# Kernel optimization log

Hardware: AMD Instinct MI355X
Metric: run time of the kernel (lower is better)

The kernel has to match this reference:

```python
import jax, jax.numpy as jnp
import numpy as np

N_ATOMS = 8192
N_PAIRS = 65536
F = 128        # n_atombasis
R = 20         # n_radialbasis
B = 5          # graph_n_blocks
EPS = 1e-8     # stability constant


def setup_inputs() -> dict:
    key = jax.random.key(0)
    ks = jax.random.split(key, 16)
    rn = lambda k, shape, s=0.05: jax.random.normal(k, shape, dtype=jnp.float32) * s
    return {
        "features": jax.random.normal(ks[0], (N_ATOMS, F), jnp.float32),
        "distances": jax.random.uniform(ks[1], (N_PAIRS,), jnp.float32, 0.5, 5.0),
        "vectors": jax.random.normal(ks[2], (N_PAIRS, 3), jnp.float32),
        "cutoffs": jax.random.uniform(ks[3], (N_PAIRS,), jnp.float32),
        "rbfs": jax.random.normal(ks[4], (N_PAIRS, R), jnp.float32),
        "filter_W": rn(ks[5], (R, B * 3 * F)),
        "filter_b": jnp.zeros((B * 3 * F,), jnp.float32),
        "int_W1": rn(ks[6], (B, F, F)),
        "int_b1": jnp.zeros((B, F), jnp.float32),
        "int_W2": rn(ks[7], (B, F, 3 * F)),
        "int_b2": jnp.zeros((B, 3 * F), jnp.float32),
        "mix_Wv": rn(ks[8], (B, F, 2 * F)),
        "mix_W1": rn(ks[9], (B, 2 * F, F)),
        "mix_b1": jnp.zeros((B, F), jnp.float32),
        "mix_W2": rn(ks[10], (B, F, 3 * F)),
        "mix_b2": jnp.zeros((B, 3 * F), jnp.float32),
        "idx_i": jax.random.randint(ks[11], (N_PAIRS,), 0, N_ATOMS),
        "idx_j": jax.random.randint(ks[12], (N_PAIRS,), 0, N_ATOMS),
    }


def reference(features, distances, vectors, cutoffs, rbfs,
              filter_W, filter_b, int_W1, int_b1, int_W2, int_b2,
              mix_Wv, mix_W1, mix_b1, mix_W2, mix_b2, idx_i, idx_j):
    n_atoms = features.shape[0]
    # Cutoff-weighted radial filters, one (3F) chunk per block: [P, B*3F]
    descriptors = (rbfs @ filter_W + filter_b) * cutoffs[:, None]
    dir_ij = vectors / distances[:, None]                       # [P, 3]

    q = features[:, None, :]                                    # [N, 1, F]
    mu = jnp.zeros((n_atoms, 3, F), dtype=features.dtype)       # [N, 3, F]

    for b in range(B):
        # --- interaction block ---
        x = jax.nn.silu(q @ int_W1[b] + int_b1[b]) @ int_W2[b] + int_b2[b]  # [N,1,3F]
        Wij = descriptors[:, None, b * 3 * F:(b + 1) * 3 * F]               # [P,1,3F]
        xj = x[idx_j] * Wij                                                 # [P,1,3F]
        muj = mu[idx_j]                                                     # [P,3,F]
        dq, dmuR, dmumu = jnp.split(xj, 3, axis=-1)                         # [P,1,F] each
        dmu = dmuR * dir_ij[:, :, None] + dmumu * muj                       # [P,3,F]
        q = q + jax.ops.segment_sum(dq, idx_i, num_segments=n_atoms)
        mu = mu + jax.ops.segment_sum(dmu, idx_i, num_segments=n_atoms)

        # --- mixing block ---
        mu_V, mu_W = jnp.split(mu @ mix_Wv[b], 2, axis=-1)                  # [N,3,F] each
        mu_Vn = jnp.sqrt(jnp.sum(mu_V ** 2, axis=-2, keepdims=True) + EPS)  # [N,1,F]
        ctx = jnp.concatenate([q, mu_Vn], axis=-1)                          # [N,1,2F]
        y = jax.nn.silu(ctx @ mix_W1[b] + mix_b1[b]) @ mix_W2[b] + mix_b2[b]
        dq_i, dmu_i, dqmu_i = jnp.split(y, 3, axis=-1)                      # [N,1,F] each
        q = q + dq_i + dqmu_i * jnp.sum(mu_V * mu_W, axis=1, keepdims=True)
        mu = mu + dmu_i * mu_W

    return q[:, 0, :], mu
```

## Files before the change

### kernel.cpp

```cpp
#include <hip/hip_runtime.h>
#include <hip/hip_bf16.h>

#define NA 8192
#define NP 65536
#define WROW 1920

typedef short short8 __attribute__((ext_vector_type(8)));
typedef short short4v __attribute__((ext_vector_type(4)));
typedef float floatx4 __attribute__((ext_vector_type(4)));

static __device__ __forceinline__ short f2bf(float f) {
    union { float f; unsigned u; } v; v.f = f;
    unsigned r = v.u + 0x7FFF + ((v.u >> 16) & 1);
    return (short)(r >> 16);
}
static __device__ __forceinline__ float bf2f(short s) {
    union { unsigned u; float f; } v;
    v.u = ((unsigned)(unsigned short)s) << 16;
    return v.f;
}
static __device__ __forceinline__ unsigned char f2fp8(float f) {
    int p = __builtin_amdgcn_cvt_pk_fp8_f32(f, 0.f, 0, false);
    return (unsigned char)(p & 0xFF);
}
static __device__ __forceinline__ float fp82f(unsigned char b) {
    return __builtin_amdgcn_cvt_f32_fp8((int)b, 0);
}
static __device__ __forceinline__ float silu(float v) {
    return v / (1.f + __expf(-v));
}

static __device__ __forceinline__ void swz(const float* __restrict__ src,
                                           short* __restrict__ dst,
                                           int K, int N, int idx) {
    int kn = K * N;
    int b = idx / kn;
    int r = idx - b * kn;
    int tile = r >> 9, li = r & 511;
    int lane = li >> 3, bb = li & 7;
    int Kt = K >> 5;
    int nt = tile / Kt, kt = tile - nt * Kt;
    int k = kt * 32 + (lane >> 4) * 8 + bb;
    int n = nt * 16 + (lane & 15);
    dst[idx] = f2bf(src[b * kn + k * N + n]);
}

__global__ __launch_bounds__(256) void k_tconv_all(const float* __restrict__ iW1,
                                                   const float* __restrict__ iW2,
                                                   const float* __restrict__ mWv,
                                                   const float* __restrict__ mW1,
                                                   const float* __restrict__ mW2,
                                                   const float* __restrict__ fW,
                                                   short* __restrict__ W1t,
                                                   short* __restrict__ W2t,
                                                   short* __restrict__ Wvt,
                                                   short* __restrict__ mW1t,
                                                   short* __restrict__ mW2t,
                                                   short* __restrict__ fWt) {
    int idx = blockIdx.x * 256 + threadIdx.x;
    if (idx < 81920)       { swz(iW1, W1t, 128, 128, idx); return; }
    idx -= 81920;
    if (idx < 245760)      { swz(iW2, W2t, 128, 384, idx); return; }
    idx -= 245760;
    if (idx < 163840)      { swz(mWv, Wvt, 128, 256, idx); return; }
    idx -= 163840;
    if (idx < 163840)      { swz(mW1, mW1t, 256, 128, idx); return; }
    idx -= 163840;
    if (idx < 245760)      { swz(mW2, mW2t, 128, 384, idx); return; }
    idx -= 245760;
    if (idx < 61440) {
        int b = idx / 12288;
        int r = idx - b * 12288;
        int nt = r >> 9;
        int li = r & 511;
        int lane = li >> 3, bb = li & 7;
        int k = (lane >> 4) * 8 + bb;
        int n = nt * 16 + (lane & 15);
        fWt[idx] = (k < 20) ? f2bf(fW[k * WROW + b * 384 + n]) : (short)0;
    }
}

__global__ __launch_bounds__(256) void k_init(const float* __restrict__ feat,
                                              float* __restrict__ q,
                                              float* __restrict__ mu,
                                              short* __restrict__ q_bf,
                                              short* __restrict__ mu_bfA,
                                              int* __restrict__ counts,
                                              int* __restrict__ cursor,
                                              float* __restrict__ cut_csr,
                                              short* __restrict__ rbf_c) {
    int idx = blockIdx.x * 256 + threadIdx.x;
    if (idx < NA * 128) { float v = feat[idx]; q[idx] = v; q_bf[idx] = f2bf(v); }
    mu[idx] = 0.f;
    mu_bfA[idx] = 0;
    if (idx < NA) { counts[idx] = 0; cursor[idx] = 0; }
    if (idx < 16) {
        cut_csr[NP + idx] = 0.f;
        #pragma unroll
        for (int k = 0; k < 32; ++k) rbf_c[(NP + idx) * 32 + k] = 0;
    }
}

__global__ __launch_bounds__(256) void k_hist(const int* __restrict__ idx_i,
                                              int* __restrict__ counts) {
    int p = blockIdx.x * 256 + threadIdx.x;
    if (p < NP) atomicAdd(&counts[idx_i[p]], 1);
}

__global__ __launch_bounds__(1024) void k_scan(const int* __restrict__ counts,
                                               int* __restrict__ offs) {
    __shared__ int sums[1024];
    int t = threadIdx.x;
    int local[8];
    int s = 0;
    #pragma unroll
    for (int k = 0; k < 8; ++k) { local[k] = s; s += counts[t * 8 + k]; }
    sums[t] = s;
    __syncthreads();
    for (int off = 1; off < 1024; off <<= 1) {
        int v = sums[t];
        int u = (t >= off) ? sums[t - off] : 0;
        __syncthreads();
        sums[t] = v + u;
        __syncthreads();
    }
    int base = (t > 0) ? sums[t - 1] : 0;
    #pragma unroll
    for (int k = 0; k < 8; ++k) offs[t * 8 + k] = base + local[k];
    if (t == 1023) offs[NA] = sums[1023];
}

__global__ __launch_bounds__(256) void k_fillprep(const int* __restrict__ idx_i,
                                                  const int* __restrict__ idx_j,
                                                  const int* __restrict__ offs,
                                                  int* __restrict__ cursor,
                                                  const float* __restrict__ cut,
                                                  const float* __restrict__ dist,
                                                  const float* __restrict__ vec,
                                                  const float* __restrict__ rbfs,
                                                  int* __restrict__ jcsr,
                                                  float* __restrict__ cut_csr,
                                                  float4* __restrict__ dir_csr,
                                                  short* __restrict__ rbf_c) {
    int p = blockIdx.x * 256 + threadIdx.x;
    if (p >= NP) return;
    int i = idx_i[p];
    int pos = atomicAdd(&cursor[i], 1);
    int e = offs[i] + pos;
    jcsr[e] = idx_j[p];
    float c = cut[p];
    cut_csr[e] = c;
    float invd = 1.f / dist[p];
    float4 d;
    d.x = vec[p * 3 + 0] * invd;
    d.y = vec[p * 3 + 1] * invd;
    d.z = vec[p * 3 + 2] * invd;
    d.w = 0.f;
    dir_csr[e] = d;
    #pragma unroll
    for (int k = 0; k < 20; ++k) rbf_c[e * 32 + k] = f2bf(rbfs[p * 20 + k] * c);
    #pragma unroll
    for (int k = 20; k < 32; ++k) rbf_c[e * 32 + k] = 0;
}

__global__ __launch_bounds__(256) void k_x(const short* __restrict__ q_bf,
                                           const short* __restrict__ W1sw,
                                           const short* __restrict__ W2sw,
                                           const float* __restrict__ b1,
                                           const float* __restrict__ b2,
                                           unsigned char* __restrict__ x_fp8) {
    __shared__ __align__(16) short qtile[16 * 136];
    __shared__ __align__(16) short hs[16 * 136];
    int t = threadIdx.x;
    int wv = t >> 6, lane = t & 63, quad = lane >> 4, l16 = lane & 15;
    int a0 = blockIdx.x * 16;

    #pragma unroll
    for (int it = 0; it < 2; ++it) {
        int c = it * 256 + t;
        int row = c >> 5, col4 = c & 31;
        *(short4v*)(qtile + row * 136 + col4 * 4) =
            *(const short4v*)(q_bf + (a0 + row) * 128 + col4 * 4);
    }
    __syncthreads();

    floatx4 acc0 = {0.f, 0.f, 0.f, 0.f}, acc1 = {0.f, 0.f, 0.f, 0.f};
    #pragma unroll
    for (int kk = 0; kk < 4; ++kk) {
        short8 a  = *(const short8*)(qtile + l16 * 136 + kk * 32 + quad * 8);
        short8 b0 = *(const short8*)(W1sw + ((wv * 2 + 0) * 4 + kk) * 512 + lane * 8);
        short8 bq = *(const short8*)(W1sw + ((wv * 2 + 1) * 4 + kk) * 512 + lane * 8);
        acc0 = __builtin_amdgcn_mfma_f32_16x16x32_bf16(a, b0, acc0, 0, 0, 0);
        acc1 = __builtin_amdgcn_mfma_f32_16x16x32_bf16(a, bq, acc1, 0, 0, 0);
    }
    __syncthreads();
    {
        int n0 = wv * 32 + l16;
        float bia0 = b1[n0], bia1 = b1[n0 + 16];
        #pragma unroll
        for (int r = 0; r < 4; ++r) {
            int m = quad * 4 + r;
            hs[m * 136 + n0]      = f2bf(silu(acc0[r] + bia0));
            hs[m * 136 + n0 + 16] = f2bf(silu(acc1[r] + bia1));
        }
    }
    __syncthreads();
    floatx4 acc[6];
    #pragma unroll
    for (int jj = 0; jj < 6; ++jj) acc[jj] = {0.f, 0.f, 0.f, 0.f};
    #pragma unroll
    for (int kk = 0; kk < 4; ++kk) {
        short8 a = *(const short8*)(hs + l16 * 136 + kk * 32 + quad * 8);
        #pragma unroll
        for (int jj = 0; jj < 6; ++jj) {
            short8 b = *(const short8*)(W2sw + ((wv * 6 + jj) * 4 + kk) * 512 + lane * 8);
            acc[jj] = __builtin_amdgcn_mfma_f32_16x16x32_bf16(a, b, acc[jj], 0, 0, 0);
        }
    }
    #pragma unroll
    for (int jj = 0; jj < 6; ++jj) {
        int n = wv * 96 + jj * 16 + l16;
        float bia = b2[n];
        #pragma unroll
        for (int r = 0; r < 4; ++r) {
            int m = quad * 4 + r;
            x_fp8[(a0 + m) * 384 + n] = f2fp8(acc[jj][r] + bia);
        }
    }
}

__global__ __launch_bounds__(256, 6) void k_gather(const unsigned char* __restrict__ x_fp8,
                                                   const short* __restrict__ mu_bfA,
                                                   const short* __restrict__ rbf_c,
                                                   const short* __restrict__ fWt,
                                                   const float* __restrict__ fbp,
                                                   const int* __restrict__ jcsr,
                                                   const float* __restrict__ cut_csr,
                                                   const float4* __restrict__ dir_csr,
                                                   const int* __restrict__ offs,
                                                   float* __restrict__ q,
                                                   float* __restrict__ mu,
                                                   short* __restrict__ q_bf,
                                                   short* __restrict__ mu_bfB) {
    __shared__ short dlds[16 * 392];
    __shared__ float pm[4 * 128];
    int i = blockIdx.x;
    int t = threadIdx.x;
    int h = t >> 7;
    int f = t & 127;
    int wv = t >> 6, lane = t & 63, quad = lane >> 4, l16 = lane & 15;
    int start = offs[i], end = offs[i + 1];
    float qa = 0.f, m0a = 0.f, m1a = 0.f, m2a = 0.f;

    for (int e0 = start; e0 < end; e0 += 16) {
        if (e0 > start) __syncthreads();
        short8 a = *(const short8*)(rbf_c + (e0 + l16) * 32 + quad * 8);
        float c0 = cut_csr[e0 + quad * 4 + 0];
        float c1 = cut_csr[e0 + quad * 4 + 1];
        float c2 = cut_csr[e0 + quad * 4 + 2];
        float c3 = cut_csr[e0 + quad * 4 + 3];
        #pragma unroll
        for (int nt = 0; nt < 6; ++nt) {
            int col = wv * 96 + nt * 16 + l16;
            short8 bfr = *(const short8*)(fWt + (wv * 6 + nt) * 512 + lane * 8);
            floatx4 z = {0.f, 0.f, 0.f, 0.f};
            floatx4 acc = __builtin_amdgcn_mfma_f32_16x16x32_bf16(a, bfr, z, 0, 0, 0);
            float fbv = fbp[col];
            dlds[(quad * 4 + 0) * 392 + col] = f2bf(acc[0] + fbv * c0);
            dlds[(quad * 4 + 1) * 392 + col] = f2bf(acc[1] + fbv * c1);
            dlds[(quad * 4 + 2) * 392 + col] = f2bf(acc[2] + fbv * c2);
            dlds[(quad * 4 + 3) * 392 + col] = f2bf(acc[3] + fbv * c3);
        }
        __syncthreads();
        int lim = (end < e0 + 16) ? end : (e0 + 16);
        int e = e0 + h;
        if (e < lim) {
            int jA = jcsr[e];
            float4 dirA = dir_csr[e];
            unsigned char aX0 = x_fp8[jA * 384 + f];
            unsigned char aX1 = x_fp8[jA * 384 + 128 + f];
            unsigned char aX2 = x_fp8[jA * 384 + 256 + f];
            short aU0 = mu_bfA[jA * 384 + f];
            short aU1 = mu_bfA[jA * 384 + 128 + f];
            short aU2 = mu_bfA[jA * 384 + 256 + f];
            for (; e < lim; e += 2) {
                float x0 = fp82f(aX0), x1 = fp82f(aX1), x2 = fp82f(aX2);
                float u0 = bf2f(aU0), u1 = bf2f(aU1), u2 = bf2f(aU2);
                float4 cdir = dirA;
                int en = e + 2;
                if (en < lim) {
                    int jn = jcsr[en];
                    dirA = dir_csr[en];
                    aX0 = x_fp8[jn * 384 + f];
                    aX1 = x_fp8[jn * 384 + 128 + f];
                    aX2 = x_fp8[jn * 384 + 256 + f];
                    aU0 = mu_bfA[jn * 384 + f];
                    aU1 = mu_bfA[jn * 384 + 128 + f];
                    aU2 = mu_bfA[jn * 384 + 256 + f];
                }
                int le = e - e0;
                float wa = bf2f(dlds[le * 392 + f]);
                float wb = bf2f(dlds[le * 392 + 128 + f]);
                float wc = bf2f(dlds[le * 392 + 256 + f]);
                qa += x0 * wa;
                float xb = x1 * wb;
                float xc = x2 * wc;
                m0a += xb * cdir.x + xc * u0;
                m1a += xb * cdir.y + xc * u1;
                m2a += xb * cdir.z + xc * u2;
            }
        }
    }
    if (h == 1) {
        pm[0 * 128 + f] = qa;
        pm[1 * 128 + f] = m0a;
        pm[2 * 128 + f] = m1a;
        pm[3 * 128 + f] = m2a;
    }
    __syncthreads();
    if (h == 0) {
        qa  += pm[0 * 128 + f];
        m0a += pm[1 * 128 + f];
        m1a += pm[2 * 128 + f];
        m2a += pm[3 * 128 + f];
        float qn = q[i * 128 + f] + qa;
        q[i * 128 + f] = qn;
        q_bf[i * 128 + f] = f2bf(qn);
        float mn0 = mu[(i * 3 + 0) * 128 + f] + m0a;
        float mn1 = mu[(i * 3 + 1) * 128 + f] + m1a;
        float mn2 = mu[(i * 3 + 2) * 128 + f] + m2a;
        mu[(i * 3 + 0) * 128 + f] = mn0;
        mu[(i * 3 + 1) * 128 + f] = mn1;
        mu[(i * 3 + 2) * 128 + f] = mn2;
        mu_bfB[(i * 3 + 0) * 128 + f] = f2bf(mn0);
        mu_bfB[(i * 3 + 1) * 128 + f] = f2bf(mn1);
        mu_bfB[(i * 3 + 2) * 128 + f] = f2bf(mn2);
    }
}

__global__ __launch_bounds__(512, 4) void k_mixx(const short* __restrict__ mu_bfB,
                                                 const short* __restrict__ Wvsw,
                                                 const short* __restrict__ q_bf_ro,
                                                 const short* __restrict__ W1sw,
                                                 const short* __restrict__ W2sw,
                                                 const float* __restrict__ b1,
                                                 const float* __restrict__ b2,
                                                 float* __restrict__ q,
                                                 float* __restrict__ mu,
                                                 short* __restrict__ q_bf,
                                                 short* __restrict__ mu_bfA,
                                                 const short* __restrict__ xW1sw,
                                                 const short* __restrict__ xW2sw,
                                                 const float* __restrict__ xb1,
                                                 const float* __restrict__ xb2,
                                                 unsigned char* __restrict__ x_fp8,
                                                 int do_x) {
    __shared__ __align__(16) char smem[51968];
    short* ms    = (short*)(smem);
    short* qtile = (short*)(smem + 13056);
    short* Vv    = (short*)(smem + 17408);
    short* hs    = (short*)(smem + 17408);
    short* Vw    = (short*)(smem + 30464);
    short* vnb   = (short*)(smem + 43520);
    short* sb    = (short*)(smem + 47872);
    int t = threadIdx.x;
    int wv = t >> 6, lane = t & 63, quad = lane >> 4, l16 = lane & 15;
    int a0 = blockIdx.x * 16;

    #pragma unroll
    for (int it = 0; it < 3; ++it) {
        int c = it * 512 + t;
        int row = c >> 5, col4 = c & 31;
        *(short4v*)(ms + row * 136 + col4 * 4) =
            *(const short4v*)(mu_bfB + (a0 * 3 + row) * 128 + col4 * 4);
    }
    {
        int row = t >> 5, col4 = t & 31;
        *(short4v*)(qtile + row * 136 + col4 * 4) =
            *(const short4v*)(q_bf_ro + (a0 + row) * 128 + col4 * 4);
    }
    __syncthreads();

    {
        floatx4 acc[3][2];
        #pragma unroll
        for (int mt = 0; mt < 3; ++mt)
            #pragma unroll
            for (int nt = 0; nt < 2; ++nt) acc[mt][nt] = {0.f, 0.f, 0.f, 0.f};
        #pragma unroll
        for (int kk = 0; kk < 4; ++kk) {
            short8 a[3];
            #pragma unroll
            for (int mt = 0; mt < 3; ++mt)
                a[mt] = *(const short8*)(ms + (mt * 16 + l16) * 136 + kk * 32 + quad * 8);
            #pragma unroll
            for (int nt = 0; nt < 2; ++nt) {
                short8 b = *(const short8*)(Wvsw + ((wv * 2 + nt) * 4 + kk) * 512 + lane * 8);
                #pragma unroll
                for (int mt = 0; mt < 3; ++mt)
                    acc[mt][nt] = __builtin_amdgcn_mfma_f32_16x16x32_bf16(a[mt], b, acc[mt][nt], 0, 0, 0);
            }
        }
        __syncthreads();
        #pragma unroll
        for (int mt = 0; mt < 3; ++mt)
            #pragma unroll
            for (int nt = 0; nt < 2; ++nt)
                #pragma unroll
                for (int r = 0; r < 4; ++r) {
                    int row = mt * 16 + quad * 4 + r;
                    int col = wv * 32 + nt * 16 + l16;
                    short v = f2bf(acc[mt][nt][r]);
                    if (col < 128) Vv[row * 136 + col] = v;
                    else           Vw[row * 136 + col - 128] = v;
                }
    }
    __syncthreads();
    #pragma unroll
    for (int k = 0; k < 4; ++k) {
        int idx = k * 512 + t;
        int a = idx >> 7, c = idx & 127;
        float v0 = bf2f(Vv[(a * 3 + 0) * 136 + c]);
        float v1 = bf2f(Vv[(a * 3 + 1) * 136 + c]);
        float v2 = bf2f(Vv[(a * 3 + 2) * 136 + c]);
        float w0 = bf2f(Vw[(a * 3 + 0) * 136 + c]);
        float w1 = bf2f(Vw[(a * 3 + 1) * 136 + c]);
        float w2 = bf2f(Vw[(a * 3 + 2) * 136 + c]);
        vnb[a * 136 + c] = f2bf(sqrtf(v0 * v0 + v1 * v1 + v2 * v2 + 1e-8f));
        sb[a * 128 + c]  = f2bf(v0 * w0 + v1 * w1 + v2 * w2);
    }
    __syncthreads();
    {
        floatx4 acc0 = {0.f, 0.f, 0.f, 0.f};
        #pragma unroll
        for (int kk = 0; kk < 8; ++kk) {
            short8 a;
            if (kk < 4)
                a = *(const short8*)(qtile + l16 * 136 + kk * 32 + quad * 8);
            else
                a = *(const short8*)(vnb + l16 * 136 + (kk - 4) * 32 + quad * 8);
            short8 b0 = *(const short8*)(W1sw + (wv * 8 + kk) * 512 + lane * 8);
            acc0 = __builtin_amdgcn_mfma_f32_16x16x32_bf16(a, b0, acc0, 0, 0, 0);
        }
        __syncthreads();
        int n0 = wv * 16 + l16;
        float bia0 = b1[n0];
        #pragma unroll
        for (int r = 0; r < 4; ++r) {
            int m = quad * 4 + r;
            hs[m * 136 + n0] = f2bf(silu(acc0[r] + bia0));
        }
    }
    __syncthreads();
    {
        floatx4 accB[3];
        #pragma unroll
        for (int c = 0; c < 3; ++c) accB[c] = {0.f, 0.f, 0.f, 0.f};
        #pragma unroll
        for (int kk = 0; kk < 4; ++kk) {
            short8 a = *(const short8*)(hs + l16 * 136 + kk * 32 + quad * 8);
            #pragma unroll
            for (int c = 0; c < 3; ++c) {
                short8 b = *(const short8*)(W2sw + ((c * 8 + wv) * 4 + kk) * 512 + lane * 8);
                accB[c] = __builtin_amdgcn_mfma_f32_16x16x32_bf16(a, b, accB[c], 0, 0, 0);
            }
        }
        int co = wv * 16 + l16;
        float bq_  = b2[co];
        float bm_  = b2[128 + co];
        float bqm_ = b2[256 + co];
        #pragma unroll
        for (int r = 0; r < 4; ++r) {
            int m = quad * 4 + r;
            int ga = a0 + m;
            float dq   = accB[0][r] + bq_;
            float dmu  = accB[1][r] + bm_;
            float dqmu = accB[2][r] + bqm_;
            float sv = bf2f(sb[m * 128 + co]);
            float qn = q[ga * 128 + co] + dq + dqmu * sv;
            q[ga * 128 + co] = qn;
            short qnb = f2bf(qn);
            q_bf[ga * 128 + co] = qnb;
            qtile[m * 136 + co] = qnb;
            #pragma unroll
            for (int d = 0; d < 3; ++d) {
                float mw = bf2f(Vw[(m * 3 + d) * 136 + co]);
                float mn = mu[(ga * 3 + d) * 128 + co] + dmu * mw;
                mu[(ga * 3 + d) * 128 + co] = mn;
                mu_bfA[(ga * 3 + d) * 128 + co] = f2bf(mn);
            }
        }
    }
    if (!do_x) return;
    __syncthreads();
    {
        floatx4 acc0 = {0.f, 0.f, 0.f, 0.f};
        #pragma unroll
        for (int kk = 0; kk < 4; ++kk) {
            short8 a  = *(const short8*)(qtile + l16 * 136 + kk * 32 + quad * 8);
            short8 b0 = *(const short8*)(xW1sw + (wv * 4 + kk) * 512 + lane * 8);
            acc0 = __builtin_amdgcn_mfma_f32_16x16x32_bf16(a, b0, acc0, 0, 0, 0);
        }
        __syncthreads();
        int n0 = wv * 16 + l16;
        float bia0 = xb1[n0];
        #pragma unroll
        for (int r = 0; r < 4; ++r) {
            int m = quad * 4 + r;
            hs[m * 136 + n0] = f2bf(silu(acc0[r] + bia0));
        }
    }
    __syncthreads();
    {
        floatx4 acc[3];
        #pragma unroll
        for (int jj = 0; jj < 3; ++jj) acc[jj] = {0.f, 0.f, 0.f, 0.f};
        #pragma unroll
        for (int kk = 0; kk < 4; ++kk) {
            short8 a = *(const short8*)(hs + l16 * 136 + kk * 32 + quad * 8);
            #pragma unroll
            for (int jj = 0; jj < 3; ++jj) {
                short8 b = *(const short8*)(xW2sw + ((wv * 3 + jj) * 4 + kk) * 512 + lane * 8);
                acc[jj] = __builtin_amdgcn_mfma_f32_16x16x32_bf16(a, b, acc[jj], 0, 0, 0);
            }
        }
        #pragma unroll
        for (int jj = 0; jj < 3; ++jj) {
            int n = wv * 48 + jj * 16 + l16;
            float bia = xb2[n];
            #pragma unroll
            for (int r = 0; r < 4; ++r) {
                int m = quad * 4 + r;
                x_fp8[(a0 + m) * 384 + n] = f2fp8(acc[jj][r] + bia);
            }
        }
    }
}

extern "C" void kernel_launch(void* const* d_in, const int* in_sizes, int n_in,
                              void* d_out, int out_size, void* d_ws, size_t ws_size,
                              hipStream_t stream) {
    const float* feat = (const float*)d_in[0];
    const float* dist = (const float*)d_in[1];
    const float* vec  = (const float*)d_in[2];
    const float* cut  = (const float*)d_in[3];
    const float* rbfs = (const float*)d_in[4];
    const float* fW   = (const float*)d_in[5];
    const float* fb   = (const float*)d_in[6];
    const float* iW1  = (const float*)d_in[7];
    const float* ib1  = (const float*)d_in[8];
    const float* iW2  = (const float*)d_in[9];
    const float* ib2  = (const float*)d_in[10];
    const float* mWv  = (const float*)d_in[11];
    const float* mW1  = (const float*)d_in[12];
    const float* mb1  = (const float*)d_in[13];
    const float* mW2  = (const float*)d_in[14];
    const float* mb2  = (const float*)d_in[15];
    const int* idx_i  = (const int*)d_in[16];
    const int* idx_j  = (const int*)d_in[17];

    float* q  = (float*)d_out;
    float* mu = (float*)d_out + NA * 128;

    char* w = (char*)d_ws;
    unsigned char* x_fp8 = (unsigned char*)(w);
    short* q_bf    = (short*)(w + 6291456);
    short* mu_bfA  = (short*)(w + 8388608);
    short* mu_bfB  = (short*)(w + 14680064);
    short* W1t     = (short*)(w + 20971520);
    short* W2t     = (short*)(w + 21135360);
    short* Wvt     = (short*)(w + 21626880);
    short* mW1t    = (short*)(w + 21954560);
    short* mW2t    = (short*)(w + 22282240);
    short* fWt     = (short*)(w + 22773760);
    int*   counts  = (int*)(w + 22896640);
    int*   cursor  = (int*)(w + 22929408);
    int*   offs    = (int*)(w + 22962176);
    int*   jcsr    = (int*)(w + 23257104);
    float* cut_csr = (float*)(w + 23519248);
    float4* dir_csr= (float4*)(w + 23781456);
    short* rbf_c   = (short*)(w + 24830032);

    k_tconv_all<<<(962560 + 255) / 256, 256, 0, stream>>>(iW1, iW2, mWv, mW1, mW2, fW,
                                                          W1t, W2t, Wvt, mW1t, mW2t, fWt);
    k_init<<<NA * 384 / 256, 256, 0, stream>>>(feat, q, mu, q_bf, mu_bfA, counts, cursor,
                                               cut_csr, rbf_c);
    k_hist<<<NP / 256, 256, 0, stream>>>(idx_i, counts);
    k_scan<<<1, 1024, 0, stream>>>(counts, offs);
    k_fillprep<<<NP / 256, 256, 0, stream>>>(idx_i, idx_j, offs, cursor, cut, dist, vec,
                                             rbfs, jcsr, cut_csr, dir_csr, rbf_c);

    k_x<<<NA / 16, 256, 0, stream>>>(q_bf, W1t, W2t, ib1, ib2, x_fp8);
    for (int b = 0; b < 5; ++b) {
        int bn = (b + 1) % 5;
        k_gather<<<NA, 256, 0, stream>>>(x_fp8, mu_bfA, rbf_c, fWt + b * 12288,
                                         fb + b * 384, jcsr, cut_csr, dir_csr,
                                         offs, q, mu, q_bf, mu_bfB);
        k_mixx<<<NA / 16, 512, 0, stream>>>(mu_bfB, Wvt + b * 32768, q_bf,
                                            mW1t + b * 32768, mW2t + b * 49152,
                                            mb1 + b * 128, mb2 + b * 384,
                                            q, mu, q_bf, mu_bfA,
                                            W1t + bn * 16384, W2t + bn * 49152,
                                            ib1 + bn * 128, ib2 + bn * 384,
                                            x_fp8, (b < 4) ? 1 : 0);
    }
}
```

Measured before the change: 429.0 us.

## Emit bf16 deltas from gather and fold residual update into mixing kernel

The gather kernel no longer reads and writes the fp32 q/mu state and its bf16 copies. It writes only bf16 deltas for q and mu. The mixing kernel now reads the fp32 state plus the deltas, forms the updated tiles itself, and applies the residual in its epilogue. This cuts the gather kernel's read-modify-write traffic, but the mixing kernel reads fp32 state and the deltas twice, and storing the aggregated deltas in bf16 adds rounding error.

```diff
diff --git a/kernel.cpp b/kernel.cpp
--- a/kernel.cpp
+++ b/kernel.cpp
@@ -238,10 +238,8 @@
                                                    const float* __restrict__ cut_csr,
                                                    const float4* __restrict__ dir_csr,
                                                    const int* __restrict__ offs,
-                                                   float* __restrict__ q,
-                                                   float* __restrict__ mu,
-                                                   short* __restrict__ q_bf,
-                                                   short* __restrict__ mu_bfB) {
+                                                   short* __restrict__ dqg,
+                                                   short* __restrict__ dmug) {
     __shared__ short dlds[16 * 392];
     __shared__ float pm[4 * 128];
     int i = blockIdx.x;
@@ -323,31 +321,24 @@
         m0a += pm[1 * 128 + f];
         m1a += pm[2 * 128 + f];
         m2a += pm[3 * 128 + f];
-        float qn = q[i * 128 + f] + qa;
-        q[i * 128 + f] = qn;
-        q_bf[i * 128 + f] = f2bf(qn);
-        float mn0 = mu[(i * 3 + 0) * 128 + f] + m0a;
-        float mn1 = mu[(i * 3 + 1) * 128 + f] + m1a;
-        float mn2 = mu[(i * 3 + 2) * 128 + f] + m2a;
-        mu[(i * 3 + 0) * 128 + f] = mn0;
-        mu[(i * 3 + 1) * 128 + f] = mn1;
-        mu[(i * 3 + 2) * 128 + f] = mn2;
-        mu_bfB[(i * 3 + 0) * 128 + f] = f2bf(mn0);
-        mu_bfB[(i * 3 + 1) * 128 + f] = f2bf(mn1);
-        mu_bfB[(i * 3 + 2) * 128 + f] = f2bf(mn2);
-    }
-}
-
-__global__ __launch_bounds__(512, 4) void k_mixx(const short* __restrict__ mu_bfB,
+        dqg[i * 128 + f]             = f2bf(qa);
+        dmug[(i * 3 + 0) * 128 + f]  = f2bf(m0a);
+        dmug[(i * 3 + 1) * 128 + f]  = f2bf(m1a);
+        dmug[(i * 3 + 2) * 128 + f]  = f2bf(m2a);
+    }
+}
+
+__global__ __launch_bounds__(512, 4) void k_mixx(const float* __restrict__ mu_ro,
+                                                 const short* __restrict__ dmug,
+                                                 const float* __restrict__ q_ro,
+                                                 const short* __restrict__ dqg,
                                                  const short* __restrict__ Wvsw,
-                                                 const short* __restrict__ q_bf_ro,
                                                  const short* __restrict__ W1sw,
                                                  const short* __restrict__ W2sw,
                                                  const float* __restrict__ b1,
                                                  const float* __restrict__ b2,
                                                  float* __restrict__ q,
                                                  float* __restrict__ mu,
-                                                 short* __restrict__ q_bf,
                                                  short* __restrict__ mu_bfA,
                                                  const short* __restrict__ xW1sw,
                                                  const short* __restrict__ xW2sw,
@@ -368,16 +359,18 @@
     int a0 = blockIdx.x * 16;
 
     #pragma unroll
-    for (int it = 0; it < 3; ++it) {
-        int c = it * 512 + t;
-        int row = c >> 5, col4 = c & 31;
-        *(short4v*)(ms + row * 136 + col4 * 4) =
-            *(const short4v*)(mu_bfB + (a0 * 3 + row) * 128 + col4 * 4);
-    }
-    {
-        int row = t >> 5, col4 = t & 31;
-        *(short4v*)(qtile + row * 136 + col4 * 4) =
-            *(const short4v*)(q_bf_ro + (a0 + row) * 128 + col4 * 4);
+    for (int k = 0; k < 12; ++k) {
+        int idx = k * 512 + t;
+        int row = idx >> 7, c = idx & 127;
+        int g = (a0 * 3 + row) * 128 + c;
+        ms[row * 136 + c] = f2bf(mu_ro[g] + bf2f(dmug[g]));
+    }
+    #pragma unroll
+    for (int k = 0; k < 4; ++k) {
+        int idx = k * 512 + t;
+        int row = idx >> 7, c = idx & 127;
+        int g = (a0 + row) * 128 + c;
+        qtile[row * 136 + c] = f2bf(q_ro[g] + bf2f(dqg[g]));
     }
     __syncthreads();
 
@@ -477,17 +470,17 @@
             float dmu  = accB[1][r] + bm_;
             float dqmu = accB[2][r] + bqm_;
             float sv = bf2f(sb[m * 128 + co]);
-            float qn = q[ga * 128 + co] + dq + dqmu * sv;
-            q[ga * 128 + co] = qn;
-            short qnb = f2bf(qn);
-            q_bf[ga * 128 + co] = qnb;
-            qtile[m * 136 + co] = qnb;
+            int gq = ga * 128 + co;
+            float qn = (q[gq] + bf2f(dqg[gq])) + dq + dqmu * sv;
+            q[gq] = qn;
+            qtile[m * 136 + co] = f2bf(qn);
             #pragma unroll
             for (int d = 0; d < 3; ++d) {
+                int gm = (ga * 3 + d) * 128 + co;
                 float mw = bf2f(Vw[(m * 3 + d) * 136 + co]);
-                float mn = mu[(ga * 3 + d) * 128 + co] + dmu * mw;
-                mu[(ga * 3 + d) * 128 + co] = mn;
-                mu_bfA[(ga * 3 + d) * 128 + co] = f2bf(mn);
+                float mn = (mu[gm] + bf2f(dmug[gm])) + dmu * mw;
+                mu[gm] = mn;
+                mu_bfA[gm] = f2bf(mn);
             }
         }
     }
@@ -564,9 +557,10 @@
 
     char* w = (char*)d_ws;
     unsigned char* x_fp8 = (unsigned char*)(w);
+    short* dqg     = (short*)(w + 3145728);
     short* q_bf    = (short*)(w + 6291456);
     short* mu_bfA  = (short*)(w + 8388608);
-    short* mu_bfB  = (short*)(w + 14680064);
+    short* dmug    = (short*)(w + 14680064);
     short* W1t     = (short*)(w + 20971520);
     short* W2t     = (short*)(w + 21135360);
     short* Wvt     = (short*)(w + 21626880);
@@ -595,11 +589,12 @@
         int bn = (b + 1) % 5;
         k_gather<<<NA, 256, 0, stream>>>(x_fp8, mu_bfA, rbf_c, fWt + b * 12288,
                                          fb + b * 384, jcsr, cut_csr, dir_csr,
-                                         offs, q, mu, q_bf, mu_bfB);
-        k_mixx<<<NA / 16, 512, 0, stream>>>(mu_bfB, Wvt + b * 32768, q_bf,
+                                         offs, dqg, dmug);
+        k_mixx<<<NA / 16, 512, 0, stream>>>(mu, dmug, q, dqg,
+                                            Wvt + b * 32768,
                                             mW1t + b * 32768, mW2t + b * 49152,
                                             mb1 + b * 128, mb2 + b * 384,
-                                            q, mu, q_bf, mu_bfA,
+                                            q, mu, mu_bfA,
                                             W1t + bn * 16384, W2t + bn * 49152,
                                             ib1 + bn * 128, ib2 + bn * 384,
                                             x_fp8, (b < 4) ? 1 : 0);
```

Result: faster. 417.7 us (-2.6%).
